# Optimization experiments

Hardware: AMD Instinct MI355X
Metric: run time of the kernel (lower is better)

Reference implementation:

```python
import jax, jax.numpy as jnp
import numpy as np

C, F, CLS, B, HW = 2048, 512, 200, 128, 14
SCALES = (4, 5, 7, 11)
EPS = 1e-5

def _pool_matrix(n, k):
    # PyTorch AdaptiveAvgPool2d bin edges: [floor(i*n/k), ceil((i+1)*n/k))
    P = np.zeros((k, n), np.float32)
    for i in range(k):
        s = (i * n) // k
        e = -((-(i + 1) * n) // k)
        P[i, s:e] = 1.0 / (e - s)
    return jnp.asarray(P)

_PMATS = [_pool_matrix(HW, k) for k in SCALES]

def _bn(x, g, b):
    # BatchNorm with batch statistics (train-mode), biased variance, eps=1e-5
    m = x.mean(0)
    v = x.var(0)
    return (x - m) * jax.lax.rsqrt(v + EPS) * g + b

def _head(h, g1, b1, w1, bi1, g2, b2, w2, bi2):
    # Sequential(BN, Linear, BN, ELU, Linear)
    h = _bn(h, g1, b1) @ w1.T + bi1
    h = jax.nn.elu(_bn(h, g2, b2))
    return h @ w2.T + bi2

def setup_inputs():
    key = jax.random.key(0)
    ks = iter(jax.random.split(key, 16))
    def rn(shape, scale=0.02):
        return jax.random.normal(next(ks), shape, jnp.float32) * scale
    d = {"x": jax.random.normal(next(ks), (B, C, HW, HW), jnp.float32)}
    d.update(g_bn_g=jnp.ones((C,)), g_bn_b=jnp.zeros((C,)), g_w=rn((4, C)), g_b=jnp.zeros((4,)))
    d.update(e_w=rn((C, C)), e_b=jnp.zeros((C,)), e_g=jnp.ones((C,)), e_bb=jnp.zeros((C,)))
    def head(p, din, dh):
        d[p + "_g1"] = jnp.ones((din,)); d[p + "_b1"] = jnp.zeros((din,))
        d[p + "_w1"] = rn((dh, din));   d[p + "_bi1"] = jnp.zeros((dh,))
        d[p + "_g2"] = jnp.ones((dh,)); d[p + "_b2"] = jnp.zeros((dh,))
        d[p + "_w2"] = rn((CLS, dh));   d[p + "_bi2"] = jnp.zeros((CLS,))
    head("hl", C, F)
    head("hh", C, F)
    head("hf", 2 * C, 2 * F)
    return d

def reference(x, g_bn_g, g_bn_b, g_w, g_b, e_w, e_b, e_g, e_bb,
              hl_g1, hl_b1, hl_w1, hl_bi1, hl_g2, hl_b2, hl_w2, hl_bi2,
              hh_g1, hh_b1, hh_w1, hh_bi1, hh_g2, hh_b2, hh_w2, hh_bi2,
              hf_g1, hf_b1, hf_w1, hf_bi1, hf_g2, hf_b2, hf_w2, hf_bi2):
    # Gate: global max pool -> BN -> ELU -> Linear -> hard gumbel-softmax (temp=1,
    # deterministic/eval: straight-through hard argmax over softmax)
    mp = x.max((2, 3))                                              # [B,C]
    logits = jax.nn.elu(_bn(mp, g_bn_g, g_bn_b)) @ g_w.T + g_b      # [B,4]
    soft = jax.nn.softmax(logits, -1)
    hard = jax.nn.one_hot(jnp.argmax(soft, -1), 4, dtype=soft.dtype)
    gw = jax.lax.stop_gradient(hard - soft) + soft                  # [B,4]
    # multi-scale adaptive avg pool (4,5,7,11) then global max per scale — fully batched
    ms = jnp.stack([jnp.einsum('ki,bcij,lj->bckl', P, x, P).max((2, 3)) for P in _PMATS], -1)  # [B,C,4]
    pool = jnp.einsum('bcs,bs->bc', ms, gw)                         # gated weighted sum
    # expert_low: 1x1 conv on 1x1 spatial == linear, then BN2d(batch stats) + ReLU
    xl = jax.nn.relu(_bn(pool @ e_w.T + e_b, e_g, e_bb))
    # NOTE: source computes expert_high(x) then overwrites with self.max(x) -> x_high = global max pool of x
    xh = mp
    xf = jnp.concatenate([xl, xh], -1)
    out_low = _head(xl, hl_g1, hl_b1, hl_w1, hl_bi1, hl_g2, hl_b2, hl_w2, hl_bi2)
    out_high = _head(xh, hh_g1, hh_b1, hh_w1, hh_bi1, hh_g2, hh_b2, hh_w2, hh_bi2)
    out = _head(xf, hf_g1, hf_b1, hf_w1, hf_bi1, hf_g2, hf_b2, hf_w2, hf_bi2)
    return (out_low, out_high, out)
```

## Files before the change

kernel.cpp:

```cpp
#include <hip/hip_runtime.h>
#include <math.h>

#define B_DIM 128
#define C_DIM 2048
#define HW2   196

typedef __attribute__((ext_vector_type(8))) short bf16x8;
typedef __attribute__((ext_vector_type(4))) float f32x4;

__device__ __forceinline__ unsigned short f2bf(float f) {
  unsigned u = __float_as_uint(f);
  u += 0x7FFFu + ((u >> 16) & 1u);
  return (unsigned short)(u >> 16);
}

__global__ __launch_bounds__(256) void pool_max_kernel(
    const float* __restrict__ x, float* __restrict__ mp, float* __restrict__ ms) {
  __shared__ float lds[4][4][208];
  const int tid  = threadIdx.x;
  const int w    = tid >> 6;
  const int lane = tid & 63;
  const int g    = lane >> 4;
  const int c    = lane & 15;
  const size_t waveBase = (size_t)blockIdx.x * 16 + w * 4;

  const float* src = x + waveBase * HW2;
  #pragma unroll
  for (int j = 0; j < 4; ++j) {
    int f = lane + 64 * j;
    if (f < 196) {
      int t = (f * 669) >> 15;
      float4 v = *(const float4*)(src + f * 4);
      *(float4*)&lds[w][t][(f - 49 * t) * 4] = v;
    }
  }

  float xv[14];
  const float* col = &lds[w][g][c];
  #pragma unroll
  for (int r = 0; r < 14; ++r) xv[r] = col[r * 14];

  float cmax = (c < 14) ? xv[0] : -INFINITY;
  #pragma unroll
  for (int r = 1; r < 14; ++r) if (c < 14) cmax = fmaxf(cmax, xv[r]);
  #pragma unroll
  for (int off = 8; off > 0; off >>= 1) cmax = fmaxf(cmax, __shfl_xor(cmax, off));

  float P[15];
  P[0] = 0.f;
  #pragma unroll
  for (int r = 0; r < 14; ++r) P[r + 1] = P[r] + xv[r];

  float sm0, sm1, sm2, sm3;

  {
    constexpr int rs[4] = {0, 3, 7, 10}, re[4] = {4, 7, 11, 14};
    const bool valid = (0x489u >> c) & 1;
    float vmax = -INFINITY;
    #pragma unroll
    for (int i = 0; i < 4; ++i) {
      float v  = P[re[i]] - P[rs[i]];
      float w2 = v + __shfl_down(v, 1);
      float w4 = w2 + __shfl_down(w2, 2);
      vmax = fmaxf(vmax, valid ? w4 : -INFINITY);
    }
    #pragma unroll
    for (int off = 8; off > 0; off >>= 1) vmax = fmaxf(vmax, __shfl_xor(vmax, off));
    sm0 = vmax * 0.0625f;
  }
  {
    constexpr int rs[5] = {0, 2, 5, 8, 11}, re[5] = {3, 6, 9, 12, 14};
    constexpr float srl[5] = {1.f/3.f, 0.25f, 0.25f, 0.25f, 1.f/3.f};
    const bool valid = (0x925u >> c) & 1;
    const bool is3   = (0x801u >> c) & 1;
    const float invc = is3 ? (1.f/3.f) : 0.25f;
    float vmax = -INFINITY;
    #pragma unroll
    for (int i = 0; i < 5; ++i) {
      float v  = P[re[i]] - P[rs[i]];
      float d1 = __shfl_down(v, 1);
      float d2 = __shfl_down(v, 2);
      float w2 = v + d1;
      float w3 = w2 + d2;
      float w4 = w2 + __shfl_down(w2, 2);
      float wv = (is3 ? w3 : w4) * invc * srl[i];
      vmax = fmaxf(vmax, valid ? wv : -INFINITY);
    }
    #pragma unroll
    for (int off = 8; off > 0; off >>= 1) vmax = fmaxf(vmax, __shfl_xor(vmax, off));
    sm1 = vmax;
  }
  {
    constexpr int rs[7] = {0, 2, 4, 6, 8, 10, 12};
    const bool valid = (0x1555u >> c) & 1;
    float vmax = -INFINITY;
    #pragma unroll
    for (int i = 0; i < 7; ++i) {
      float v  = P[rs[i] + 2] - P[rs[i]];
      float w2 = v + __shfl_down(v, 1);
      vmax = fmaxf(vmax, valid ? w2 : -INFINITY);
    }
    #pragma unroll
    for (int off = 8; off > 0; off >>= 1) vmax = fmaxf(vmax, __shfl_xor(vmax, off));
    sm2 = vmax * 0.25f;
  }
  {
    constexpr int rs[11] = {0, 1, 2, 3, 5, 6, 7, 8, 10, 11, 12};
    constexpr int re[11] = {2, 3, 4, 6, 7, 8, 9, 11, 12, 13, 14};
    constexpr float srl[11] = {0.5f, 0.5f, 0.5f, 1.f/3.f, 0.5f, 0.5f, 0.5f,
                               1.f/3.f, 0.5f, 0.5f, 0.5f};
    const bool valid = (0x1DEFu >> c) & 1;
    const bool is3   = (0x108u >> c) & 1;
    const float invc = is3 ? (1.f/3.f) : 0.5f;
    float vmax = -INFINITY;
    #pragma unroll
    for (int i = 0; i < 11; ++i) {
      float v  = P[re[i]] - P[rs[i]];
      float d1 = __shfl_down(v, 1);
      float d2 = __shfl_down(v, 2);
      float w2 = v + d1;
      float w3 = w2 + d2;
      float wv = (is3 ? w3 : w2) * invc * srl[i];
      vmax = fmaxf(vmax, valid ? wv : -INFINITY);
    }
    #pragma unroll
    for (int off = 8; off > 0; off >>= 1) vmax = fmaxf(vmax, __shfl_xor(vmax, off));
    sm3 = vmax;
  }

  if (c == 0) {
    size_t T = waveBase + g;
    mp[T] = cmax;
    *(float4*)&ms[T * 4] = make_float4(sm0, sm1, sm2, sm3);
  }
}

__global__ __launch_bounds__(256) void statsmp_kernel(
    const float* __restrict__ mp,
    const float* __restrict__ hh_g1, const float* __restrict__ hh_b1,
    const float* __restrict__ hf_g1, const float* __restrict__ hf_b1,
    float* __restrict__ mean_mp, float* __restrict__ rstd_mp,
    float* __restrict__ s_h, float* __restrict__ t_h,
    float* __restrict__ sf2, float* __restrict__ tf2) {
  const int ci = threadIdx.x & 15;
  const int g  = threadIdx.x >> 4;
  const int c  = blockIdx.x * 16 + ci;
  float s = 0.f, q = 0.f;
  #pragma unroll
  for (int r = 0; r < 8; ++r) {
    float v = mp[(size_t)(g * 8 + r) * C_DIM + c];
    s += v; q += v * v;
  }
  __shared__ float ss[16][16], qq[16][16];
  ss[g][ci] = s; qq[g][ci] = q;
  __syncthreads();
  if (g == 0) {
    float S = 0.f, Q = 0.f;
    #pragma unroll
    for (int j = 0; j < 16; ++j) { S += ss[j][ci]; Q += qq[j][ci]; }
    float m = S * (1.f / B_DIM);
    float var = Q * (1.f / B_DIM) - m * m;
    if (var < 0.f) var = 0.f;
    float r = rsqrtf(var + 1e-5f);
    mean_mp[c] = m; rstd_mp[c] = r;
    float a = r * hh_g1[c];        s_h[c] = a; t_h[c] = hh_b1[c] - m * a;
    float b = r * hf_g1[2048 + c]; sf2[c] = b; tf2[c] = hf_b1[2048 + c] - m * b;
  }
}

__global__ void gate_select_kernel(
    const float* __restrict__ mp,
    const float* __restrict__ mean, const float* __restrict__ rstd,
    const float* __restrict__ gg, const float* __restrict__ gb,
    const float* __restrict__ gw, const float* __restrict__ gbias,
    const float* __restrict__ ms, float* __restrict__ pool) {
  const int b = blockIdx.x;
  const int t = threadIdx.x;
  float s0 = 0.f, s1 = 0.f, s2 = 0.f, s3 = 0.f;
  for (int c = t; c < C_DIM; c += 256) {
    float v = mp[(size_t)b * C_DIM + c];
    float xn = (v - mean[c]) * rstd[c] * gg[c] + gb[c];
    float e = xn > 0.f ? xn : expm1f(xn);
    s0 += e * gw[c];
    s1 += e * gw[C_DIM + c];
    s2 += e * gw[2 * C_DIM + c];
    s3 += e * gw[3 * C_DIM + c];
  }
  __shared__ float red[4][256];
  __shared__ int ssel;
  red[0][t] = s0; red[1][t] = s1; red[2][t] = s2; red[3][t] = s3;
  __syncthreads();
  for (int st = 128; st > 0; st >>= 1) {
    if (t < st) {
      red[0][t] += red[0][t + st];
      red[1][t] += red[1][t + st];
      red[2][t] += red[2][t + st];
      red[3][t] += red[3][t + st];
    }
    __syncthreads();
  }
  if (t == 0) {
    float best = red[0][0] + gbias[0];
    int bi = 0;
    for (int j = 1; j < 4; ++j) {
      float l = red[j][0] + gbias[j];
      if (l > best) { best = l; bi = j; }
    }
    ssel = bi;
  }
  __syncthreads();
  const int sel = ssel;
  for (int c = t; c < C_DIM; c += 256)
    pool[(size_t)b * C_DIM + c] = ms[((size_t)b * C_DIM + c) * 4 + sel];
}

__global__ __launch_bounds__(256) void gemm_e_mfma_kernel(
    const float* __restrict__ A, const float* __restrict__ W,
    float* __restrict__ P) {
  __shared__ __align__(16) short As[64 * 64];
  __shared__ __align__(16) short Bs[64 * 64];
  const int t = threadIdx.x;
  const int n0 = blockIdx.x << 6;
  const int m0 = blockIdx.y << 6;
  const int kbeg = blockIdx.z << 8;

  const int rowS = t >> 2, koff = (t & 3) << 4;

  const int lane = t & 63, wav = t >> 6;
  const int r = lane & 15, kb = lane >> 4;
  int aoff[2], boff[2][4];
  #pragma unroll
  for (int kk = 0; kk < 2; ++kk) {
    int row = wav * 16 + r;
    aoff[kk] = row * 128 + ((((kk << 2) + kb) ^ (row & 7)) << 4);
    #pragma unroll
    for (int ni = 0; ni < 4; ++ni) {
      int cl = ni * 16 + r;
      boff[kk][ni] = cl * 128 + ((((kk << 2) + kb) ^ (cl & 7)) << 4);
    }
  }

  f32x4 acc[4];
  #pragma unroll
  for (int ni = 0; ni < 4; ++ni) acc[ni] = (f32x4){0.f, 0.f, 0.f, 0.f};

  for (int kt = 0; kt < 256; kt += 64) {
    const int kg = kbeg + kt + koff;
    const float4* ap = (const float4*)&A[(size_t)(m0 + rowS) * 2048 + kg];
    const float4* bp = (const float4*)&W[(size_t)(n0 + rowS) * 2048 + kg];
    float4 fa[4], fb[4];
    #pragma unroll
    for (int j = 0; j < 4; ++j) fa[j] = ap[j];
    #pragma unroll
    for (int j = 0; j < 4; ++j) fb[j] = bp[j];
    __syncthreads();
    #pragma unroll
    for (int j = 0; j < 2; ++j) {
      bf16x8 va, vb;
      va[0] = (short)f2bf(fa[2*j].x);   va[1] = (short)f2bf(fa[2*j].y);
      va[2] = (short)f2bf(fa[2*j].z);   va[3] = (short)f2bf(fa[2*j].w);
      va[4] = (short)f2bf(fa[2*j+1].x); va[5] = (short)f2bf(fa[2*j+1].y);
      va[6] = (short)f2bf(fa[2*j+1].z); va[7] = (short)f2bf(fa[2*j+1].w);
      vb[0] = (short)f2bf(fb[2*j].x);   vb[1] = (short)f2bf(fb[2*j].y);
      vb[2] = (short)f2bf(fb[2*j].z);   vb[3] = (short)f2bf(fb[2*j].w);
      vb[4] = (short)f2bf(fb[2*j+1].x); vb[5] = (short)f2bf(fb[2*j+1].y);
      vb[6] = (short)f2bf(fb[2*j+1].z); vb[7] = (short)f2bf(fb[2*j+1].w);
      int slot = (koff >> 3) + j;
      *(bf16x8*)((char*)As + rowS * 128 + ((slot ^ (rowS & 7)) << 4)) = va;
      *(bf16x8*)((char*)Bs + rowS * 128 + ((slot ^ (rowS & 7)) << 4)) = vb;
    }
    __syncthreads();
    #pragma unroll
    for (int kk = 0; kk < 2; ++kk) {
      bf16x8 a0 = *(bf16x8*)((char*)As + aoff[kk]);
      bf16x8 b0 = *(bf16x8*)((char*)Bs + boff[kk][0]);
      bf16x8 b1 = *(bf16x8*)((char*)Bs + boff[kk][1]);
      bf16x8 b2 = *(bf16x8*)((char*)Bs + boff[kk][2]);
      bf16x8 b3 = *(bf16x8*)((char*)Bs + boff[kk][3]);
      acc[0] = __builtin_amdgcn_mfma_f32_16x16x32_bf16(a0, b0, acc[0], 0, 0, 0);
      acc[1] = __builtin_amdgcn_mfma_f32_16x16x32_bf16(a0, b1, acc[1], 0, 0, 0);
      acc[2] = __builtin_amdgcn_mfma_f32_16x16x32_bf16(a0, b2, acc[2], 0, 0, 0);
      acc[3] = __builtin_amdgcn_mfma_f32_16x16x32_bf16(a0, b3, acc[3], 0, 0, 0);
    }
  }

  float* Pz = P + ((size_t)blockIdx.z << 18);
  #pragma unroll
  for (int ni = 0; ni < 4; ++ni) {
    int cl = n0 + ni * 16 + r;
    int row = m0 + wav * 16 + kb * 4;
    #pragma unroll
    for (int g2 = 0; g2 < 4; ++g2)
      Pz[(size_t)(row + g2) * 2048 + cl] = acc[ni][g2];
  }
}

__global__ __launch_bounds__(256) void expert_fused_kernel(
    const float* __restrict__ Pe, const float* __restrict__ e_b,
    const float* __restrict__ e_g, const float* __restrict__ e_bb,
    const float* __restrict__ hl_g1, const float* __restrict__ hl_b1,
    const float* __restrict__ hf_g1, const float* __restrict__ hf_b1,
    float* __restrict__ xl,
    float* __restrict__ s_l, float* __restrict__ t_l,
    float* __restrict__ sf1, float* __restrict__ tf1) {
  const int ci = threadIdx.x & 15;
  const int g  = threadIdx.x >> 4;
  const int c  = blockIdx.x * 16 + ci;
  float v[8];
  float s = 0.f, q = 0.f;
  const float bias = e_b[c];
  #pragma unroll
  for (int r = 0; r < 8; ++r) {
    const size_t row = g * 8 + r;
    float acc = bias;
    #pragma unroll
    for (int z = 0; z < 8; ++z)
      acc += Pe[((size_t)z << 18) + row * 2048 + c];
    v[r] = acc; s += acc; q += acc * acc;
  }
  __shared__ float ss[16][16], qq[16][16];
  __shared__ float sm[16], sr[16];
  ss[g][ci] = s; qq[g][ci] = q;
  __syncthreads();
  if (g == 0) {
    float S = 0.f, Q = 0.f;
    #pragma unroll
    for (int j = 0; j < 16; ++j) { S += ss[j][ci]; Q += qq[j][ci]; }
    float m = S * (1.f / B_DIM);
    float var = Q * (1.f / B_DIM) - m * m;
    if (var < 0.f) var = 0.f;
    sm[ci] = m; sr[ci] = rsqrtf(var + 1e-5f);
  }
  __syncthreads();
  const float m = sm[ci], rst = sr[ci];
  const float eg = e_g[c], eb2 = e_bb[c];
  float s2 = 0.f, q2 = 0.f;
  #pragma unroll
  for (int r = 0; r < 8; ++r) {
    float xv = fmaxf((v[r] - m) * rst * eg + eb2, 0.f);
    xl[(size_t)(g * 8 + r) * 2048 + c] = xv;
    s2 += xv; q2 += xv * xv;
  }
  __syncthreads();
  ss[g][ci] = s2; qq[g][ci] = q2;
  __syncthreads();
  if (g == 0) {
    float S = 0.f, Q = 0.f;
    #pragma unroll
    for (int j = 0; j < 16; ++j) { S += ss[j][ci]; Q += qq[j][ci]; }
    float mm = S * (1.f / B_DIM);
    float var = Q * (1.f / B_DIM) - mm * mm;
    if (var < 0.f) var = 0.f;
    float rr = rsqrtf(var + 1e-5f);
    float a = rr * hl_g1[c]; s_l[c] = a; t_l[c] = hl_b1[c] - mm * a;
    float b = rr * hf_g1[c]; sf1[c] = b; tf1[c] = hf_b1[c] - mm * b;
  }
}

__global__ __launch_bounds__(256) void gemm_w1_mfma_kernel(
    const float* __restrict__ xl, const float* __restrict__ mp,
    const float* __restrict__ s_l, const float* __restrict__ t_l,
    const float* __restrict__ s_h, const float* __restrict__ t_h,
    const float* __restrict__ sf1, const float* __restrict__ tf1,
    const float* __restrict__ sf2, const float* __restrict__ tf2,
    const float* __restrict__ hl_w1, const float* __restrict__ hh_w1,
    const float* __restrict__ hf_w1,
    float* __restrict__ P_l, float* __restrict__ P_h, float* __restrict__ P_f) {
  __shared__ __align__(16) short As[64 * 64];
  __shared__ __align__(16) short Bs[64 * 64];
  const int jx = blockIdx.x;
  const int m0 = blockIdx.y << 6;
  const int z  = blockIdx.z;
  const float *A, *S, *T, *Wt;
  float* P;
  int N, Kdim, n0, kA0, kW0, Kc;
  if (jx < 8) {
    N = 512; Kdim = 2048; Kc = 256; Wt = hl_w1; n0 = jx << 6;
    kW0 = z * 256; kA0 = kW0; A = xl; S = s_l; T = t_l;
    P = P_l + ((size_t)z << 16);
  } else if (jx < 16) {
    N = 512; Kdim = 2048; Kc = 256; Wt = hh_w1; n0 = (jx - 8) << 6;
    kW0 = z * 256; kA0 = kW0; A = mp; S = s_h; T = t_h;
    P = P_h + ((size_t)z << 16);
  } else {
    N = 1024; Kdim = 4096; Kc = 512; Wt = hf_w1; n0 = (jx - 16) << 6;
    kW0 = z * 512;
    if (kW0 >= 2048) { A = mp; S = sf2; T = tf2; kA0 = kW0 - 2048; }
    else             { A = xl; S = sf1; T = tf1; kA0 = kW0; }
    P = P_f + ((size_t)z << 17);
  }
  const int t = threadIdx.x;
  const int rowS = t >> 2, koff = (t & 3) << 4;

  const int lane = t & 63, wav = t >> 6;
  const int r = lane & 15, kb = lane >> 4;
  int aoff[2], boff[2][4];
  #pragma unroll
  for (int kk = 0; kk < 2; ++kk) {
    int row = wav * 16 + r;
    aoff[kk] = row * 128 + ((((kk << 2) + kb) ^ (row & 7)) << 4);
    #pragma unroll
    for (int ni = 0; ni < 4; ++ni) {
      int cl = ni * 16 + r;
      boff[kk][ni] = cl * 128 + ((((kk << 2) + kb) ^ (cl & 7)) << 4);
    }
  }

  f32x4 acc[4];
  #pragma unroll
  for (int ni = 0; ni < 4; ++ni) acc[ni] = (f32x4){0.f, 0.f, 0.f, 0.f};

  for (int kt = 0; kt < Kc; kt += 64) {
    const int ka = kA0 + kt + koff;
    const float4* ap = (const float4*)&A[(size_t)(m0 + rowS) * 2048 + ka];
    const float4* sp = (const float4*)&S[ka];
    const float4* tp = (const float4*)&T[ka];
    const float4* bp = (const float4*)&Wt[(size_t)(n0 + rowS) * Kdim + kW0 + kt + koff];
    float4 fa[4], fb[4];
    #pragma unroll
    for (int j = 0; j < 4; ++j) fa[j] = ap[j];
    #pragma unroll
    for (int j = 0; j < 4; ++j) {
      float4 s4 = sp[j], t4 = tp[j];
      fa[j].x = fmaf(fa[j].x, s4.x, t4.x);
      fa[j].y = fmaf(fa[j].y, s4.y, t4.y);
      fa[j].z = fmaf(fa[j].z, s4.z, t4.z);
      fa[j].w = fmaf(fa[j].w, s4.w, t4.w);
    }
    #pragma unroll
    for (int j = 0; j < 4; ++j) fb[j] = bp[j];
    __syncthreads();
    #pragma unroll
    for (int j = 0; j < 2; ++j) {
      bf16x8 va, vb;
      va[0] = (short)f2bf(fa[2*j].x);   va[1] = (short)f2bf(fa[2*j].y);
      va[2] = (short)f2bf(fa[2*j].z);   va[3] = (short)f2bf(fa[2*j].w);
      va[4] = (short)f2bf(fa[2*j+1].x); va[5] = (short)f2bf(fa[2*j+1].y);
      va[6] = (short)f2bf(fa[2*j+1].z); va[7] = (short)f2bf(fa[2*j+1].w);
      vb[0] = (short)f2bf(fb[2*j].x);   vb[1] = (short)f2bf(fb[2*j].y);
      vb[2] = (short)f2bf(fb[2*j].z);   vb[3] = (short)f2bf(fb[2*j].w);
      vb[4] = (short)f2bf(fb[2*j+1].x); vb[5] = (short)f2bf(fb[2*j+1].y);
      vb[6] = (short)f2bf(fb[2*j+1].z); vb[7] = (short)f2bf(fb[2*j+1].w);
      int slot = (koff >> 3) + j;
      *(bf16x8*)((char*)As + rowS * 128 + ((slot ^ (rowS & 7)) << 4)) = va;
      *(bf16x8*)((char*)Bs + rowS * 128 + ((slot ^ (rowS & 7)) << 4)) = vb;
    }
    __syncthreads();
    #pragma unroll
    for (int kk = 0; kk < 2; ++kk) {
      bf16x8 a0 = *(bf16x8*)((char*)As + aoff[kk]);
      bf16x8 b0 = *(bf16x8*)((char*)Bs + boff[kk][0]);
      bf16x8 b1 = *(bf16x8*)((char*)Bs + boff[kk][1]);
      bf16x8 b2 = *(bf16x8*)((char*)Bs + boff[kk][2]);
      bf16x8 b3 = *(bf16x8*)((char*)Bs + boff[kk][3]);
      acc[0] = __builtin_amdgcn_mfma_f32_16x16x32_bf16(a0, b0, acc[0], 0, 0, 0);
      acc[1] = __builtin_amdgcn_mfma_f32_16x16x32_bf16(a0, b1, acc[1], 0, 0, 0);
      acc[2] = __builtin_amdgcn_mfma_f32_16x16x32_bf16(a0, b2, acc[2], 0, 0, 0);
      acc[3] = __builtin_amdgcn_mfma_f32_16x16x32_bf16(a0, b3, acc[3], 0, 0, 0);
    }
  }

  #pragma unroll
  for (int ni = 0; ni < 4; ++ni) {
    int cl = n0 + ni * 16 + r;
    int row = m0 + wav * 16 + kb * 4;
    #pragma unroll
    for (int g2 = 0; g2 < 4; ++g2)
      P[(size_t)(row + g2) * N + cl] = acc[ni][g2];
  }
}

__global__ __launch_bounds__(256) void heads_fused_kernel(
    const float* __restrict__ P_l, const float* __restrict__ P_h,
    const float* __restrict__ P_f,
    const float* __restrict__ bl1, const float* __restrict__ bh1,
    const float* __restrict__ bf1,
    const float* __restrict__ g2l, const float* __restrict__ b2l,
    const float* __restrict__ g2h, const float* __restrict__ b2h,
    const float* __restrict__ g2f, const float* __restrict__ b2f,
    float* __restrict__ a2_l, float* __restrict__ a2_h, float* __restrict__ a2_f) {
  const int ci = threadIdx.x & 15;
  const int g  = threadIdx.x >> 4;
  const int cj = blockIdx.x * 16 + ci;
  const float *P, *bi, *g2, *b2;
  float* out;
  int N, cc;
  if (cj < 512)       { P = P_l; bi = bl1; g2 = g2l; b2 = b2l; out = a2_l; N = 512;  cc = cj; }
  else if (cj < 1024) { P = P_h; bi = bh1; g2 = g2h; b2 = b2h; out = a2_h; N = 512;  cc = cj - 512; }
  else                { P = P_f; bi = bf1; g2 = g2f; b2 = b2f; out = a2_f; N = 1024; cc = cj - 1024; }
  const size_t sstride = (size_t)N * 128;
  float v[8];
  float s = 0.f, q = 0.f;
  const float bias = bi[cc];
  #pragma unroll
  for (int r = 0; r < 8; ++r) {
    const size_t row = g * 8 + r;
    float acc = bias;
    #pragma unroll
    for (int z = 0; z < 8; ++z)
      acc += P[(size_t)z * sstride + row * N + cc];
    v[r] = acc; s += acc; q += acc * acc;
  }
  __shared__ float ss[16][16], qq[16][16];
  __shared__ float sm[16], sr[16];
  ss[g][ci] = s; qq[g][ci] = q;
  __syncthreads();
  if (g == 0) {
    float S = 0.f, Q = 0.f;
    #pragma unroll
    for (int j = 0; j < 16; ++j) { S += ss[j][ci]; Q += qq[j][ci]; }
    float m = S * (1.f / B_DIM);
    float var = Q * (1.f / B_DIM) - m * m;
    if (var < 0.f) var = 0.f;
    sm[ci] = m; sr[ci] = rsqrtf(var + 1e-5f);
  }
  __syncthreads();
  const float m = sm[ci], rr = sr[ci];
  const float gg = g2[cc], bb = b2[cc];
  #pragma unroll
  for (int r = 0; r < 8; ++r) {
    float xn = (v[r] - m) * rr * gg + bb;
    out[(size_t)(g * 8 + r) * N + cc] = xn > 0.f ? xn : expm1f(xn);
  }
}

__global__ __launch_bounds__(256) void gemm_w2_kernel(
    const float* __restrict__ a2_l, const float* __restrict__ a2_h,
    const float* __restrict__ a2_f,
    const float* __restrict__ hl_w2, const float* __restrict__ hh_w2,
    const float* __restrict__ hf_w2,
    float* __restrict__ Pw) {
  const int jx = blockIdx.x;
  const int z  = blockIdx.z;
  const float *A, *Wt;
  int K, Kc, pOff, n0;
  if (jx < 4)      { A = a2_l; Wt = hl_w2; K = 512;  Kc = 64;  pOff = 0;     n0 = jx << 6; }
  else if (jx < 8) { A = a2_h; Wt = hh_w2; K = 512;  Kc = 64;  pOff = 25600; n0 = (jx - 4) << 6; }
  else             { A = a2_f; Wt = hf_w2; K = 1024; Kc = 128; pOff = 51200; n0 = (jx - 8) << 6; }
  const int kbeg = z * Kc;
  const int m0 = blockIdx.y << 6;
  __shared__ float As[32][68];
  __shared__ float Bs[32][68];
  const int t = threadIdx.x;
  const int lr = t >> 3;
  const int lk4 = (t & 7) << 2;
  const int tx = t & 15, ty = t >> 4;
  float acc[4][4] = {{0.f}};
  const float4 z4 = make_float4(0.f, 0.f, 0.f, 0.f);
  for (int k0 = kbeg; k0 < kbeg + Kc; k0 += 32) {
    float4 a0 = *(const float4*)&A[(size_t)(m0 + lr) * K + k0 + lk4];
    float4 a1 = *(const float4*)&A[(size_t)(m0 + lr + 32) * K + k0 + lk4];
    int n1 = n0 + lr, n2 = n0 + lr + 32;
    float4 b0 = (n1 < 200) ? *(const float4*)&Wt[(size_t)n1 * K + k0 + lk4] : z4;
    float4 b1 = (n2 < 200) ? *(const float4*)&Wt[(size_t)n2 * K + k0 + lk4] : z4;
    __syncthreads();
    As[lk4 + 0][lr] = a0.x; As[lk4 + 1][lr] = a0.y; As[lk4 + 2][lr] = a0.z; As[lk4 + 3][lr] = a0.w;
    As[lk4 + 0][lr + 32] = a1.x; As[lk4 + 1][lr + 32] = a1.y; As[lk4 + 2][lr + 32] = a1.z; As[lk4 + 3][lr + 32] = a1.w;
    Bs[lk4 + 0][lr] = b0.x; Bs[lk4 + 1][lr] = b0.y; Bs[lk4 + 2][lr] = b0.z; Bs[lk4 + 3][lr] = b0.w;
    Bs[lk4 + 0][lr + 32] = b1.x; Bs[lk4 + 1][lr + 32] = b1.y; Bs[lk4 + 2][lr + 32] = b1.z; Bs[lk4 + 3][lr + 32] = b1.w;
    __syncthreads();
    #pragma unroll
    for (int kk = 0; kk < 32; ++kk) {
      float4 av = *(const float4*)&As[kk][ty << 2];
      float4 bv = *(const float4*)&Bs[kk][tx << 2];
      acc[0][0] = fmaf(av.x, bv.x, acc[0][0]); acc[0][1] = fmaf(av.x, bv.y, acc[0][1]);
      acc[0][2] = fmaf(av.x, bv.z, acc[0][2]); acc[0][3] = fmaf(av.x, bv.w, acc[0][3]);
      acc[1][0] = fmaf(av.y, bv.x, acc[1][0]); acc[1][1] = fmaf(av.y, bv.y, acc[1][1]);
      acc[1][2] = fmaf(av.y, bv.z, acc[1][2]); acc[1][3] = fmaf(av.y, bv.w, acc[1][3]);
      acc[2][0] = fmaf(av.z, bv.x, acc[2][0]); acc[2][1] = fmaf(av.z, bv.y, acc[2][1]);
      acc[2][2] = fmaf(av.z, bv.z, acc[2][2]); acc[2][3] = fmaf(av.z, bv.w, acc[2][3]);
      acc[3][0] = fmaf(av.w, bv.x, acc[3][0]); acc[3][1] = fmaf(av.w, bv.y, acc[3][1]);
      acc[3][2] = fmaf(av.w, bv.z, acc[3][2]); acc[3][3] = fmaf(av.w, bv.w, acc[3][3]);
    }
  }
  float* Pz = Pw + (size_t)z * 76800 + pOff;
  #pragma unroll
  for (int i = 0; i < 4; ++i) {
    int m = m0 + (ty << 2) + i;
    #pragma unroll
    for (int j = 0; j < 4; ++j) {
      int n = n0 + (tx << 2) + j;
      if (n < 200) Pz[(size_t)m * 200 + n] = acc[i][j];
    }
  }
}

__global__ void reduce_out_kernel(const float* __restrict__ P,
                                  const float* __restrict__ bl,
                                  const float* __restrict__ bh,
                                  const float* __restrict__ bf,
                                  float* __restrict__ out) {
  int i = blockIdx.x * 256 + threadIdx.x;
  if (i >= 76800) return;
  int job = i / 25600;
  int n = (i - job * 25600) % 200;
  float s = (job == 0) ? bl[n] : (job == 1) ? bh[n] : bf[n];
  for (int z = 0; z < 8; ++z) s += P[(size_t)z * 76800 + i];
  out[i] = s;
}

extern "C" void kernel_launch(void* const* d_in, const int* in_sizes, int n_in,
                              void* d_out, int out_size, void* d_ws, size_t ws_size,
                              hipStream_t stream) {
  const float* x      = (const float*)d_in[0];
  const float* g_bn_g = (const float*)d_in[1];
  const float* g_bn_b = (const float*)d_in[2];
  const float* g_w    = (const float*)d_in[3];
  const float* g_b    = (const float*)d_in[4];
  const float* e_w    = (const float*)d_in[5];
  const float* e_b    = (const float*)d_in[6];
  const float* e_g    = (const float*)d_in[7];
  const float* e_bb   = (const float*)d_in[8];
  const float* hl_g1  = (const float*)d_in[9];
  const float* hl_b1  = (const float*)d_in[10];
  const float* hl_w1  = (const float*)d_in[11];
  const float* hl_bi1 = (const float*)d_in[12];
  const float* hl_g2  = (const float*)d_in[13];
  const float* hl_b2  = (const float*)d_in[14];
  const float* hl_w2  = (const float*)d_in[15];
  const float* hl_bi2 = (const float*)d_in[16];
  const float* hh_g1  = (const float*)d_in[17];
  const float* hh_b1  = (const float*)d_in[18];
  const float* hh_w1  = (const float*)d_in[19];
  const float* hh_bi1 = (const float*)d_in[20];
  const float* hh_g2  = (const float*)d_in[21];
  const float* hh_b2  = (const float*)d_in[22];
  const float* hh_w2  = (const float*)d_in[23];
  const float* hh_bi2 = (const float*)d_in[24];
  const float* hf_g1  = (const float*)d_in[25];
  const float* hf_b1  = (const float*)d_in[26];
  const float* hf_w1  = (const float*)d_in[27];
  const float* hf_bi1 = (const float*)d_in[28];
  const float* hf_g2  = (const float*)d_in[29];
  const float* hf_b2  = (const float*)d_in[30];
  const float* hf_w2  = (const float*)d_in[31];
  const float* hf_bi2 = (const float*)d_in[32];
  float* out = (float*)d_out;

  float* W = (float*)d_ws;
  const size_t BC = (size_t)B_DIM * C_DIM;
  float* mp   = W;
  float* ms   = mp + BC;
  float* pool = ms + BC * 4;
  float* xl   = pool + BC;
  float* a2_l = xl + BC;
  float* a2_h = a2_l + 128 * 512;
  float* a2_f = a2_h + 128 * 512;
  float* st   = a2_f + 128 * 1024;
  float* mean_mp = st;           float* rstd_mp = st + 2048;
  float* s_h  = st + 2 * 2048;   float* t_h  = st + 3 * 2048;
  float* sf2  = st + 4 * 2048;   float* tf2  = st + 5 * 2048;
  float* s_l  = st + 6 * 2048;   float* t_l  = st + 7 * 2048;
  float* sf1  = st + 8 * 2048;   float* tf1  = st + 9 * 2048;
  float* P_e  = st + 10 * 2048;
  float* P_l2 = P_e + 8 * BC;
  float* P_hh = P_l2 + (size_t)8 * 65536;
  float* P_f  = P_hh + (size_t)8 * 65536;
  float* P_w2 = P_e;

  pool_max_kernel<<<16384, 256, 0, stream>>>(x, mp, ms);

  statsmp_kernel<<<128, 256, 0, stream>>>(mp, hh_g1, hh_b1, hf_g1, hf_b1,
                                          mean_mp, rstd_mp, s_h, t_h, sf2, tf2);

  gate_select_kernel<<<128, 256, 0, stream>>>(mp, mean_mp, rstd_mp, g_bn_g, g_bn_b,
                                              g_w, g_b, ms, pool);

  gemm_e_mfma_kernel<<<dim3(32, 2, 8), 256, 0, stream>>>(pool, e_w, P_e);

  expert_fused_kernel<<<128, 256, 0, stream>>>(P_e, e_b, e_g, e_bb,
                                               hl_g1, hl_b1, hf_g1, hf_b1,
                                               xl, s_l, t_l, sf1, tf1);

  gemm_w1_mfma_kernel<<<dim3(32, 2, 8), 256, 0, stream>>>(
      xl, mp, s_l, t_l, s_h, t_h, sf1, tf1, sf2, tf2,
      hl_w1, hh_w1, hf_w1, P_l2, P_hh, P_f);

  heads_fused_kernel<<<128, 256, 0, stream>>>(
      P_l2, P_hh, P_f, hl_bi1, hh_bi1, hf_bi1,
      hl_g2, hl_b2, hh_g2, hh_b2, hf_g2, hf_b2,
      a2_l, a2_h, a2_f);

  gemm_w2_kernel<<<dim3(12, 2, 8), 256, 0, stream>>>(
      a2_l, a2_h, a2_f, hl_w2, hh_w2, hf_w2, P_w2);

  reduce_out_kernel<<<300, 256, 0, stream>>>(P_w2, hl_bi2, hh_bi2, hf_bi2, out);
}
```

Baseline: 130.8 us.

## Merge stats+gate and w2 GEMM+reduce into cooperative kernels with grid sync

Result: slower. 255.8 us (+95.5%).

```diff
diff --git a/kernel.cpp b/kernel.cpp
--- a/kernel.cpp
+++ b/kernel.cpp
@@ -1,5 +1,8 @@
 #include <hip/hip_runtime.h>
+#include <hip/hip_cooperative_groups.h>
 #include <math.h>
+
+namespace cg = cooperative_groups;
 
 #define B_DIM 128
 #define C_DIM 2048
@@ -135,83 +138,86 @@
   }
 }
 
-__global__ __launch_bounds__(256) void statsmp_kernel(
+__global__ __launch_bounds__(256) void stats_gate_kernel(
     const float* __restrict__ mp,
     const float* __restrict__ hh_g1, const float* __restrict__ hh_b1,
     const float* __restrict__ hf_g1, const float* __restrict__ hf_b1,
+    const float* __restrict__ gg, const float* __restrict__ gb,
+    const float* __restrict__ gw, const float* __restrict__ gbias,
+    const float* __restrict__ ms,
     float* __restrict__ mean_mp, float* __restrict__ rstd_mp,
     float* __restrict__ s_h, float* __restrict__ t_h,
-    float* __restrict__ sf2, float* __restrict__ tf2) {
-  const int ci = threadIdx.x & 15;
-  const int g  = threadIdx.x >> 4;
-  const int c  = blockIdx.x * 16 + ci;
-  float s = 0.f, q = 0.f;
-  #pragma unroll
-  for (int r = 0; r < 8; ++r) {
-    float v = mp[(size_t)(g * 8 + r) * C_DIM + c];
-    s += v; q += v * v;
-  }
-  __shared__ float ss[16][16], qq[16][16];
-  ss[g][ci] = s; qq[g][ci] = q;
-  __syncthreads();
-  if (g == 0) {
-    float S = 0.f, Q = 0.f;
-    #pragma unroll
-    for (int j = 0; j < 16; ++j) { S += ss[j][ci]; Q += qq[j][ci]; }
-    float m = S * (1.f / B_DIM);
-    float var = Q * (1.f / B_DIM) - m * m;
-    if (var < 0.f) var = 0.f;
-    float r = rsqrtf(var + 1e-5f);
-    mean_mp[c] = m; rstd_mp[c] = r;
-    float a = r * hh_g1[c];        s_h[c] = a; t_h[c] = hh_b1[c] - m * a;
-    float b = r * hf_g1[2048 + c]; sf2[c] = b; tf2[c] = hf_b1[2048 + c] - m * b;
-  }
-}
-
-__global__ void gate_select_kernel(
-    const float* __restrict__ mp,
-    const float* __restrict__ mean, const float* __restrict__ rstd,
-    const float* __restrict__ gg, const float* __restrict__ gb,
-    const float* __restrict__ gw, const float* __restrict__ gbias,
-    const float* __restrict__ ms, float* __restrict__ pool) {
-  const int b = blockIdx.x;
-  const int t = threadIdx.x;
-  float s0 = 0.f, s1 = 0.f, s2 = 0.f, s3 = 0.f;
-  for (int c = t; c < C_DIM; c += 256) {
-    float v = mp[(size_t)b * C_DIM + c];
-    float xn = (v - mean[c]) * rstd[c] * gg[c] + gb[c];
-    float e = xn > 0.f ? xn : expm1f(xn);
-    s0 += e * gw[c];
-    s1 += e * gw[C_DIM + c];
-    s2 += e * gw[2 * C_DIM + c];
-    s3 += e * gw[3 * C_DIM + c];
-  }
-  __shared__ float red[4][256];
-  __shared__ int ssel;
-  red[0][t] = s0; red[1][t] = s1; red[2][t] = s2; red[3][t] = s3;
-  __syncthreads();
-  for (int st = 128; st > 0; st >>= 1) {
-    if (t < st) {
-      red[0][t] += red[0][t + st];
-      red[1][t] += red[1][t + st];
-      red[2][t] += red[2][t + st];
-      red[3][t] += red[3][t + st];
-    }
+    float* __restrict__ sf2, float* __restrict__ tf2,
+    float* __restrict__ pool) {
+  {
+    const int ci = threadIdx.x & 15;
+    const int g  = threadIdx.x >> 4;
+    const int c  = blockIdx.x * 16 + ci;
+    float s = 0.f, q = 0.f;
+    #pragma unroll
+    for (int r = 0; r < 8; ++r) {
+      float v = mp[(size_t)(g * 8 + r) * C_DIM + c];
+      s += v; q += v * v;
+    }
+    __shared__ float ss[16][16], qq[16][16];
+    ss[g][ci] = s; qq[g][ci] = q;
     __syncthreads();
-  }
-  if (t == 0) {
-    float best = red[0][0] + gbias[0];
-    int bi = 0;
-    for (int j = 1; j < 4; ++j) {
-      float l = red[j][0] + gbias[j];
-      if (l > best) { best = l; bi = j; }
-    }
-    ssel = bi;
-  }
-  __syncthreads();
-  const int sel = ssel;
-  for (int c = t; c < C_DIM; c += 256)
-    pool[(size_t)b * C_DIM + c] = ms[((size_t)b * C_DIM + c) * 4 + sel];
+    if (g == 0) {
+      float S = 0.f, Q = 0.f;
+      #pragma unroll
+      for (int j = 0; j < 16; ++j) { S += ss[j][ci]; Q += qq[j][ci]; }
+      float m = S * (1.f / B_DIM);
+      float var = Q * (1.f / B_DIM) - m * m;
+      if (var < 0.f) var = 0.f;
+      float r = rsqrtf(var + 1e-5f);
+      mean_mp[c] = m; rstd_mp[c] = r;
+      float a = r * hh_g1[c];        s_h[c] = a; t_h[c] = hh_b1[c] - m * a;
+      float b = r * hf_g1[2048 + c]; sf2[c] = b; tf2[c] = hf_b1[2048 + c] - m * b;
+    }
+  }
+  __threadfence();
+  cg::this_grid().sync();
+
+  {
+    const int b = blockIdx.x;
+    const int t = threadIdx.x;
+    float s0 = 0.f, s1 = 0.f, s2 = 0.f, s3 = 0.f;
+    for (int c = t; c < C_DIM; c += 256) {
+      float v = mp[(size_t)b * C_DIM + c];
+      float xn = (v - mean_mp[c]) * rstd_mp[c] * gg[c] + gb[c];
+      float e = xn > 0.f ? xn : expm1f(xn);
+      s0 += e * gw[c];
+      s1 += e * gw[C_DIM + c];
+      s2 += e * gw[2 * C_DIM + c];
+      s3 += e * gw[3 * C_DIM + c];
+    }
+    __shared__ float red[4][256];
+    __shared__ int ssel;
+    red[0][t] = s0; red[1][t] = s1; red[2][t] = s2; red[3][t] = s3;
+    __syncthreads();
+    for (int st = 128; st > 0; st >>= 1) {
+      if (t < st) {
+        red[0][t] += red[0][t + st];
+        red[1][t] += red[1][t + st];
+        red[2][t] += red[2][t + st];
+        red[3][t] += red[3][t + st];
+      }
+      __syncthreads();
+    }
+    if (t == 0) {
+      float best = red[0][0] + gbias[0];
+      int bi = 0;
+      for (int j = 1; j < 4; ++j) {
+        float l = red[j][0] + gbias[j];
+        if (l > best) { best = l; bi = j; }
+      }
+      ssel = bi;
+    }
+    __syncthreads();
+    const int sel = ssel;
+    for (int c = t; c < C_DIM; c += 256)
+      pool[(size_t)b * C_DIM + c] = ms[((size_t)b * C_DIM + c) * 4 + sel];
+  }
 }
 
 __global__ __launch_bounds__(256) void gemm_e_mfma_kernel(
@@ -524,79 +530,83 @@
   }
 }
 
-__global__ __launch_bounds__(256) void gemm_w2_kernel(
+__global__ __launch_bounds__(256) void w2_reduce_kernel(
     const float* __restrict__ a2_l, const float* __restrict__ a2_h,
     const float* __restrict__ a2_f,
     const float* __restrict__ hl_w2, const float* __restrict__ hh_w2,
     const float* __restrict__ hf_w2,
-    float* __restrict__ Pw) {
-  const int jx = blockIdx.x;
-  const int z  = blockIdx.z;
-  const float *A, *Wt;
-  int K, Kc, pOff, n0;
-  if (jx < 4)      { A = a2_l; Wt = hl_w2; K = 512;  Kc = 64;  pOff = 0;     n0 = jx << 6; }
-  else if (jx < 8) { A = a2_h; Wt = hh_w2; K = 512;  Kc = 64;  pOff = 25600; n0 = (jx - 4) << 6; }
-  else             { A = a2_f; Wt = hf_w2; K = 1024; Kc = 128; pOff = 51200; n0 = (jx - 8) << 6; }
-  const int kbeg = z * Kc;
-  const int m0 = blockIdx.y << 6;
+    const float* __restrict__ bl2, const float* __restrict__ bh2,
+    const float* __restrict__ bf2,
+    float* __restrict__ Pw, float* __restrict__ out) {
   __shared__ float As[32][68];
   __shared__ float Bs[32][68];
-  const int t = threadIdx.x;
-  const int lr = t >> 3;
-  const int lk4 = (t & 7) << 2;
-  const int tx = t & 15, ty = t >> 4;
-  float acc[4][4] = {{0.f}};
-  const float4 z4 = make_float4(0.f, 0.f, 0.f, 0.f);
-  for (int k0 = kbeg; k0 < kbeg + Kc; k0 += 32) {
-    float4 a0 = *(const float4*)&A[(size_t)(m0 + lr) * K + k0 + lk4];
-    float4 a1 = *(const float4*)&A[(size_t)(m0 + lr + 32) * K + k0 + lk4];
-    int n1 = n0 + lr, n2 = n0 + lr + 32;
-    float4 b0 = (n1 < 200) ? *(const float4*)&Wt[(size_t)n1 * K + k0 + lk4] : z4;
-    float4 b1 = (n2 < 200) ? *(const float4*)&Wt[(size_t)n2 * K + k0 + lk4] : z4;
-    __syncthreads();
-    As[lk4 + 0][lr] = a0.x; As[lk4 + 1][lr] = a0.y; As[lk4 + 2][lr] = a0.z; As[lk4 + 3][lr] = a0.w;
-    As[lk4 + 0][lr + 32] = a1.x; As[lk4 + 1][lr + 32] = a1.y; As[lk4 + 2][lr + 32] = a1.z; As[lk4 + 3][lr + 32] = a1.w;
-    Bs[lk4 + 0][lr] = b0.x; Bs[lk4 + 1][lr] = b0.y; Bs[lk4 + 2][lr] = b0.z; Bs[lk4 + 3][lr] = b0.w;
-    Bs[lk4 + 0][lr + 32] = b1.x; Bs[lk4 + 1][lr + 32] = b1.y; Bs[lk4 + 2][lr + 32] = b1.z; Bs[lk4 + 3][lr + 32] = b1.w;
-    __syncthreads();
-    #pragma unroll
-    for (int kk = 0; kk < 32; ++kk) {
-      float4 av = *(const float4*)&As[kk][ty << 2];
-      float4 bv = *(const float4*)&Bs[kk][tx << 2];
-      acc[0][0] = fmaf(av.x, bv.x, acc[0][0]); acc[0][1] = fmaf(av.x, bv.y, acc[0][1]);
-      acc[0][2] = fmaf(av.x, bv.z, acc[0][2]); acc[0][3] = fmaf(av.x, bv.w, acc[0][3]);
-      acc[1][0] = fmaf(av.y, bv.x, acc[1][0]); acc[1][1] = fmaf(av.y, bv.y, acc[1][1]);
-      acc[1][2] = fmaf(av.y, bv.z, acc[1][2]); acc[1][3] = fmaf(av.y, bv.w, acc[1][3]);
-      acc[2][0] = fmaf(av.z, bv.x, acc[2][0]); acc[2][1] = fmaf(av.z, bv.y, acc[2][1]);
-      acc[2][2] = fmaf(av.z, bv.z, acc[2][2]); acc[2][3] = fmaf(av.z, bv.w, acc[2][3]);
-      acc[3][0] = fmaf(av.w, bv.x, acc[3][0]); acc[3][1] = fmaf(av.w, bv.y, acc[3][1]);
-      acc[3][2] = fmaf(av.w, bv.z, acc[3][2]); acc[3][3] = fmaf(av.w, bv.w, acc[3][3]);
-    }
-  }
-  float* Pz = Pw + (size_t)z * 76800 + pOff;
-  #pragma unroll
-  for (int i = 0; i < 4; ++i) {
-    int m = m0 + (ty << 2) + i;
-    #pragma unroll
-    for (int j = 0; j < 4; ++j) {
-      int n = n0 + (tx << 2) + j;
-      if (n < 200) Pz[(size_t)m * 200 + n] = acc[i][j];
-    }
-  }
-}
-
-__global__ void reduce_out_kernel(const float* __restrict__ P,
-                                  const float* __restrict__ bl,
-                                  const float* __restrict__ bh,
-                                  const float* __restrict__ bf,
-                                  float* __restrict__ out) {
-  int i = blockIdx.x * 256 + threadIdx.x;
-  if (i >= 76800) return;
-  int job = i / 25600;
-  int n = (i - job * 25600) % 200;
-  float s = (job == 0) ? bl[n] : (job == 1) ? bh[n] : bf[n];
-  for (int z = 0; z < 8; ++z) s += P[(size_t)z * 76800 + i];
-  out[i] = s;
+  const int bid = blockIdx.x;
+  if (bid < 192) {
+    const int jx = bid % 12;
+    const int rest = bid / 12;
+    const int m0 = (rest & 1) << 6;
+    const int z  = rest >> 1;
+    const float *A, *Wt;
+    int K, Kc, pOff, n0;
+    if (jx < 4)      { A = a2_l; Wt = hl_w2; K = 512;  Kc = 64;  pOff = 0;     n0 = jx << 6; }
+    else if (jx < 8) { A = a2_h; Wt = hh_w2; K = 512;  Kc = 64;  pOff = 25600; n0 = (jx - 4) << 6; }
+    else             { A = a2_f; Wt = hf_w2; K = 1024; Kc = 128; pOff = 51200; n0 = (jx - 8) << 6; }
+    const int kbeg = z * Kc;
+    const int t = threadIdx.x;
+    const int lr = t >> 3;
+    const int lk4 = (t & 7) << 2;
+    const int tx = t & 15, ty = t >> 4;
+    float acc[4][4] = {{0.f}};
+    const float4 z4 = make_float4(0.f, 0.f, 0.f, 0.f);
+    for (int k0 = kbeg; k0 < kbeg + Kc; k0 += 32) {
+      float4 a0 = *(const float4*)&A[(size_t)(m0 + lr) * K + k0 + lk4];
+      float4 a1 = *(const float4*)&A[(size_t)(m0 + lr + 32) * K + k0 + lk4];
+      int n1 = n0 + lr, n2 = n0 + lr + 32;
+      float4 b0 = (n1 < 200) ? *(const float4*)&Wt[(size_t)n1 * K + k0 + lk4] : z4;
+      float4 b1 = (n2 < 200) ? *(const float4*)&Wt[(size_t)n2 * K + k0 + lk4] : z4;
+      __syncthreads();
+      As[lk4 + 0][lr] = a0.x; As[lk4 + 1][lr] = a0.y; As[lk4 + 2][lr] = a0.z; As[lk4 + 3][lr] = a0.w;
+      As[lk4 + 0][lr + 32] = a1.x; As[lk4 + 1][lr + 32] = a1.y; As[lk4 + 2][lr + 32] = a1.z; As[lk4 + 3][lr + 32] = a1.w;
+      Bs[lk4 + 0][lr] = b0.x; Bs[lk4 + 1][lr] = b0.y; Bs[lk4 + 2][lr] = b0.z; Bs[lk4 + 3][lr] = b0.w;
+      Bs[lk4 + 0][lr + 32] = b1.x; Bs[lk4 + 1][lr + 32] = b1.y; Bs[lk4 + 2][lr + 32] = b1.z; Bs[lk4 + 3][lr + 32] = b1.w;
+      __syncthreads();
+      #pragma unroll
+      for (int kk = 0; kk < 32; ++kk) {
+        float4 av = *(const float4*)&As[kk][ty << 2];
+        float4 bv = *(const float4*)&Bs[kk][tx << 2];
+        acc[0][0] = fmaf(av.x, bv.x, acc[0][0]); acc[0][1] = fmaf(av.x, bv.y, acc[0][1]);
+        acc[0][2] = fmaf(av.x, bv.z, acc[0][2]); acc[0][3] = fmaf(av.x, bv.w, acc[0][3]);
+        acc[1][0] = fmaf(av.y, bv.x, acc[1][0]); acc[1][1] = fmaf(av.y, bv.y, acc[1][1]);
+        acc[1][2] = fmaf(av.y, bv.z, acc[1][2]); acc[1][3] = fmaf(av.y, bv.w, acc[1][3]);
+        acc[2][0] = fmaf(av.z, bv.x, acc[2][0]); acc[2][1] = fmaf(av.z, bv.y, acc[2][1]);
+        acc[2][2] = fmaf(av.z, bv.z, acc[2][2]); acc[2][3] = fmaf(av.z, bv.w, acc[2][3]);
+        acc[3][0] = fmaf(av.w, bv.x, acc[3][0]); acc[3][1] = fmaf(av.w, bv.y, acc[3][1]);
+        acc[3][2] = fmaf(av.w, bv.z, acc[3][2]); acc[3][3] = fmaf(av.w, bv.w, acc[3][3]);
+      }
+    }
+    float* Pz = Pw + (size_t)z * 76800 + pOff;
+    #pragma unroll
+    for (int i = 0; i < 4; ++i) {
+      int m = m0 + (ty << 2) + i;
+      #pragma unroll
+      for (int j = 0; j < 4; ++j) {
+        int n = n0 + (tx << 2) + j;
+        if (n < 200) Pz[(size_t)m * 200 + n] = acc[i][j];
+      }
+    }
+  }
+  __threadfence();
+  cg::this_grid().sync();
+
+  {
+    int i = bid * 256 + threadIdx.x;
+    int job = i / 25600;
+    int n = (i - job * 25600) % 200;
+    float s = (job == 0) ? bl2[n] : (job == 1) ? bh2[n] : bf2[n];
+    #pragma unroll
+    for (int z = 0; z < 8; ++z) s += Pw[(size_t)z * 76800 + i];
+    out[i] = s;
+  }
 }
 
 extern "C" void kernel_launch(void* const* d_in, const int* in_sizes, int n_in,
@@ -660,11 +670,13 @@
 
   pool_max_kernel<<<16384, 256, 0, stream>>>(x, mp, ms);
 
-  statsmp_kernel<<<128, 256, 0, stream>>>(mp, hh_g1, hh_b1, hf_g1, hf_b1,
-                                          mean_mp, rstd_mp, s_h, t_h, sf2, tf2);
-
-  gate_select_kernel<<<128, 256, 0, stream>>>(mp, mean_mp, rstd_mp, g_bn_g, g_bn_b,
-                                              g_w, g_b, ms, pool);
+  {
+    void* args[] = {&mp, &hh_g1, &hh_b1, &hf_g1, &hf_b1,
+                    &g_bn_g, &g_bn_b, &g_w, &g_b, &ms,
+                    &mean_mp, &rstd_mp, &s_h, &t_h, &sf2, &tf2, &pool};
+    hipLaunchCooperativeKernel((const void*)stats_gate_kernel,
+                               dim3(128), dim3(256), args, 0, stream);
+  }
 
   gemm_e_mfma_kernel<<<dim3(32, 2, 8), 256, 0, stream>>>(pool, e_w, P_e);
 
@@ -681,8 +693,10 @@
       hl_g2, hl_b2, hh_g2, hh_b2, hf_g2, hf_b2,
       a2_l, a2_h, a2_f);
 
-  gemm_w2_kernel<<<dim3(12, 2, 8), 256, 0, stream>>>(
-      a2_l, a2_h, a2_f, hl_w2, hh_w2, hf_w2, P_w2);
-
-  reduce_out_kernel<<<300, 256, 0, stream>>>(P_w2, hl_bi2, hh_bi2, hf_bi2, out);
-}
+  {
+    void* args[] = {&a2_l, &a2_h, &a2_f, &hl_w2, &hh_w2, &hf_w2,
+                    &hl_bi2, &hh_bi2, &hf_bi2, &P_w2, &out};
+    hipLaunchCooperativeKernel((const void*)w2_reduce_kernel,
+                               dim3(300), dim3(256), args, 0, stream);
+  }
+}
```
